# Kernel tuning notes

Hardware: AMD Instinct MI355X
Metric: run time of the kernel (lower is better)

## Reference

```python
import jax, jax.numpy as jnp
import numpy as np

NB_KERNEL = 100
DIM_PER_KERNEL = 5


def setup_inputs() -> dict:
    key = jax.random.key(0)
    k1, k2 = jax.random.split(key)
    B, F = 1024, 1024
    x = jax.random.normal(k1, (B, F), dtype=jnp.float32)
    T = jax.random.normal(k2, (F, NB_KERNEL * DIM_PER_KERNEL), dtype=jnp.float32)
    return {"x": x, "T": T}


def reference(x, T):
    B = x.shape[0]
    # project: [B, F] @ [F, K*D] -> [B, K, D]
    m = (x @ T).reshape(B, NB_KERNEL, DIM_PER_KERNEL)
    # pairwise L1 distance over D between all batch rows: [B, K, B]
    # diffs[i, k, d, j] = m[i, k, d] - m[j, k, d]
    diffs = m[:, :, :, None] - jnp.transpose(m, (1, 2, 0))[None, :, :, :]
    l1 = jnp.sum(jnp.abs(diffs), axis=2)  # [B, K, B]
    # exp-kernel similarity summed across batch (includes self term exp(0)=1)
    feat = jnp.sum(jnp.exp(-l1), axis=2)  # [B, K]
    return jnp.concatenate([x, feat], axis=1)  # [B, F + K]
```

## Files before the change

kernel.cpp:

```cpp
#include <hip/hip_runtime.h>
#include <hip/hip_bf16.h>
#include <math.h>

#define B_SZ   1024
#define F_SZ   1024
#define NKER   100
#define DKER   5
#define CCOLS  (NKER * DKER)
#define OUTW   (F_SZ + NKER)
#define LOG2E_F 1.44269504088896340736f

typedef __attribute__((ext_vector_type(8))) short bf16x8;
typedef __attribute__((ext_vector_type(4))) float f32x4;

__device__ __forceinline__ float exp2_hw(float x) {
    float r;
    asm("v_exp_f32 %0, %1" : "=v"(r) : "v"(x));
    return r;
}
__device__ __forceinline__ unsigned cvt_pk_bf16(float lo, float hi) {
    unsigned r;
    asm("v_cvt_pk_bf16_f32 %0, %1, %2" : "=v"(r) : "v"(lo), "v"(hi));
    return r;
}

__global__ __launch_bounds__(256) void init_kernel(const float* __restrict__ x,
                                                   float* __restrict__ out) {
    const int row = blockIdx.x;
    const int t = threadIdx.x;
    const float4 v = *reinterpret_cast<const float4*>(&x[row * F_SZ + t * 4]);
    *reinterpret_cast<float4*>(&out[row * OUTW + t * 4]) = v;
}

#define NCT 32
#define NJT (B_SZ / 16)

__global__ __launch_bounds__(256) void gemm_wave_kernel(const float* __restrict__ x,
                                                        const float* __restrict__ T,
                                                        float* __restrict__ mt) {
    const int tid = threadIdx.x;
    const int l = tid & 63;
    const int wv = tid >> 6;
    const int tile = blockIdx.x * 4 + wv;
    const int ct = tile & (NCT - 1);
    const int jt = tile >> 5;
    const int c0 = ct * 16, j0 = jt * 16;

    const int lr = l & 15;
    const int lk = (l >> 4) * 8;

    const int cA = c0 + lr;
    const int cL = (cA < CCOLS) ? cA : (CCOLS - 1);
    const int jB = j0 + lr;

    const float* ap = T + (size_t)lk * CCOLS + cL;
    const float* bp = x + (size_t)jB * F_SZ + lk;

    f32x4 acc = {0.f, 0.f, 0.f, 0.f};

    #pragma unroll 2
    for (int s = 0; s < F_SZ / 32; ++s) {
        const float a0 = ap[0 * CCOLS], a1 = ap[1 * CCOLS];
        const float a2 = ap[2 * CCOLS], a3 = ap[3 * CCOLS];
        const float a4 = ap[4 * CCOLS], a5 = ap[5 * CCOLS];
        const float a6 = ap[6 * CCOLS], a7 = ap[7 * CCOLS];
        const float4 b0 = *reinterpret_cast<const float4*>(bp);
        const float4 b1 = *reinterpret_cast<const float4*>(bp + 4);
        ap += 32 * CCOLS;
        bp += 32;

        union { unsigned u[4]; bf16x8 v; } A, B;
        A.u[0] = cvt_pk_bf16(a0, a1);
        A.u[1] = cvt_pk_bf16(a2, a3);
        A.u[2] = cvt_pk_bf16(a4, a5);
        A.u[3] = cvt_pk_bf16(a6, a7);
        B.u[0] = cvt_pk_bf16(b0.x, b0.y);
        B.u[1] = cvt_pk_bf16(b0.z, b0.w);
        B.u[2] = cvt_pk_bf16(b1.x, b1.y);
        B.u[3] = cvt_pk_bf16(b1.z, b1.w);

        acc = __builtin_amdgcn_mfma_f32_16x16x32_bf16(A.v, B.v, acc, 0, 0, 0);
    }

    const int jst = j0 + lr;
    const int cst = c0 + (l >> 4) * 4;
    #pragma unroll
    for (int q = 0; q < 4; ++q) {
        const int c = cst + q;
        if (c < CCOLS) mt[c * B_SZ + jst] = acc[q] * LOG2E_F;
    }
}

#define PJC 128

__global__ __launch_bounds__(64) void pair_kernel(const float* __restrict__ mt,
                                                  float* __restrict__ out) {
    __shared__ float mj[DKER * PJC];
    const int tid = threadIdx.x;
    const int i = blockIdx.x * 64 + tid;
    const int k = blockIdx.y;
    const int cb = k * DKER;

    const float a0 = mt[(cb + 0) * B_SZ + i];
    const float a1 = mt[(cb + 1) * B_SZ + i];
    const float a2 = mt[(cb + 2) * B_SZ + i];
    const float a3 = mt[(cb + 3) * B_SZ + i];
    const float a4 = mt[(cb + 4) * B_SZ + i];

    float acc = 0.f;
    for (int jc = 0; jc < B_SZ; jc += PJC) {
        __syncthreads();
        #pragma unroll
        for (int r = 0; r < DKER * PJC / 64; ++r) {
            const int t2 = r * 64 + tid;
            const int d = t2 >> 7;
            const int jr = t2 & (PJC - 1);
            mj[d * PJC + jr] = mt[(cb + d) * B_SZ + jc + jr];
        }
        __syncthreads();

        #pragma unroll 4
        for (int jb = 0; jb < PJC / 4; ++jb) {
            const float4 q0 = *reinterpret_cast<const float4*>(&mj[0 * PJC + jb * 4]);
            const float4 q1 = *reinterpret_cast<const float4*>(&mj[1 * PJC + jb * 4]);
            const float4 q2 = *reinterpret_cast<const float4*>(&mj[2 * PJC + jb * 4]);
            const float4 q3 = *reinterpret_cast<const float4*>(&mj[3 * PJC + jb * 4]);
            const float4 q4 = *reinterpret_cast<const float4*>(&mj[4 * PJC + jb * 4]);
#define DOJ(C) { \
            const float d0 = a0 - q0.C; \
            const float d1 = a1 - q1.C; \
            const float d2 = a2 - q2.C; \
            const float d3 = a3 - q3.C; \
            const float d4 = a4 - q4.C; \
            const float p01 = fabsf(d0) + fabsf(d1); \
            const float p23 = fabsf(d2) + fabsf(d3); \
            const float p234 = p23 + fabsf(d4); \
            acc += exp2_hw(-p01 - p234); }
            DOJ(x) DOJ(y) DOJ(z) DOJ(w)
#undef DOJ
        }
    }

    out[i * OUTW + F_SZ + k] = acc;
}

extern "C" void kernel_launch(void* const* d_in, const int* in_sizes, int n_in,
                              void* d_out, int out_size, void* d_ws, size_t ws_size,
                              hipStream_t stream) {
    const float* x = (const float*)d_in[0];
    const float* T = (const float*)d_in[1];
    float* out = (float*)d_out;
    float* mt = (float*)d_ws;

    init_kernel<<<dim3(B_SZ), 256, 0, stream>>>(x, out);
    gemm_wave_kernel<<<dim3(NCT * NJT / 4), 256, 0, stream>>>(x, T, mt);
    pair_kernel<<<dim3(B_SZ / 64, NKER), 64, 0, stream>>>(mt, out);
}
```

Before: 135.9 us.

## Share GEMM tiles via LDS with split-K and widen pair kernel blocks

The GEMM now gives each 512-thread block a 32x32 output tile. Operands are staged as bf16 in shared memory so four waves reuse them, and the K dimension is split across two half-blocks whose partial sums are combined through LDS. This removes the redundant, uncoalesced global loads of T that each wave issued separately. The pair kernel now uses 256 threads: it loads the full 5x1024 column slice into LDS once, each wave handles a quarter of the j range, and the partial sums are reduced in shared memory. The cost is more barriers and more LDS use per block, which may lower occupancy.

```diff
diff --git a/kernel.cpp b/kernel.cpp
--- a/kernel.cpp
+++ b/kernel.cpp
@@ -32,116 +32,127 @@
     *reinterpret_cast<float4*>(&out[row * OUTW + t * 4]) = v;
 }
 
-#define NCT 32
-#define NJT (B_SZ / 16)
+#define GAPAD 40
 
-__global__ __launch_bounds__(256) void gemm_wave_kernel(const float* __restrict__ x,
-                                                        const float* __restrict__ T,
-                                                        float* __restrict__ mt) {
+__global__ __launch_bounds__(512) void gemm_block_kernel(const float* __restrict__ x,
+                                                         const float* __restrict__ T,
+                                                         float* __restrict__ mt) {
+    __shared__ short Al[2][32][GAPAD];
+    __shared__ short Bl[2][32][GAPAD];
+    __shared__ float red[4][64][4];
     const int tid = threadIdx.x;
     const int l = tid & 63;
-    const int wv = tid >> 6;
-    const int tile = blockIdx.x * 4 + wv;
-    const int ct = tile & (NCT - 1);
-    const int jt = tile >> 5;
-    const int c0 = ct * 16, j0 = jt * 16;
+    const int w = tid >> 6;
+    const int h = tid >> 8;
+    const int ht = tid & 255;
+    const int c0 = blockIdx.x * 32;
+    const int j0 = blockIdx.y * 32;
+    const int fh = h * (F_SZ / 2);
 
-    const int lr = l & 15;
-    const int lk = (l >> 4) * 8;
+    const int sac = ht & 31;
+    const int sak = (ht >> 5) * 4;
+    const int cldA = (c0 + sac < CCOLS) ? (c0 + sac) : (CCOLS - 1);
+    const int sbj = ht >> 3;
+    const int sbk = (ht & 7) * 4;
 
-    const int cA = c0 + lr;
-    const int cL = (cA < CCOLS) ? cA : (CCOLS - 1);
-    const int jB = j0 + lr;
-
-    const float* ap = T + (size_t)lk * CCOLS + cL;
-    const float* bp = x + (size_t)jB * F_SZ + lk;
+    const int q = w & 3;
+    const int cq = (q & 1) * 16;
+    const int jq = (q >> 1) * 16;
+    const int fr = (l >> 4) * 8;
+    const int ar = cq + (l & 15);
+    const int br = jq + (l & 15);
 
     f32x4 acc = {0.f, 0.f, 0.f, 0.f};
 
-    #pragma unroll 2
-    for (int s = 0; s < F_SZ / 32; ++s) {
-        const float a0 = ap[0 * CCOLS], a1 = ap[1 * CCOLS];
-        const float a2 = ap[2 * CCOLS], a3 = ap[3 * CCOLS];
-        const float a4 = ap[4 * CCOLS], a5 = ap[5 * CCOLS];
-        const float a6 = ap[6 * CCOLS], a7 = ap[7 * CCOLS];
-        const float4 b0 = *reinterpret_cast<const float4*>(bp);
-        const float4 b1 = *reinterpret_cast<const float4*>(bp + 4);
-        ap += 32 * CCOLS;
-        bp += 32;
-
-        union { unsigned u[4]; bf16x8 v; } A, B;
-        A.u[0] = cvt_pk_bf16(a0, a1);
-        A.u[1] = cvt_pk_bf16(a2, a3);
-        A.u[2] = cvt_pk_bf16(a4, a5);
-        A.u[3] = cvt_pk_bf16(a6, a7);
-        B.u[0] = cvt_pk_bf16(b0.x, b0.y);
-        B.u[1] = cvt_pk_bf16(b0.z, b0.w);
-        B.u[2] = cvt_pk_bf16(b1.x, b1.y);
-        B.u[3] = cvt_pk_bf16(b1.z, b1.w);
-
-        acc = __builtin_amdgcn_mfma_f32_16x16x32_bf16(A.v, B.v, acc, 0, 0, 0);
+    for (int s = 0; s < 16; ++s) {
+        const int fb = fh + s * 32;
+        const float a0 = T[(fb + sak + 0) * CCOLS + cldA];
+        const float a1 = T[(fb + sak + 1) * CCOLS + cldA];
+        const float a2 = T[(fb + sak + 2) * CCOLS + cldA];
+        const float a3 = T[(fb + sak + 3) * CCOLS + cldA];
+        const float4 b = *reinterpret_cast<const float4*>(&x[(j0 + sbj) * F_SZ + fb + sbk]);
+        if (s) __syncthreads();
+        {
+            uint2 aw; aw.x = cvt_pk_bf16(a0, a1); aw.y = cvt_pk_bf16(a2, a3);
+            *reinterpret_cast<uint2*>(&Al[h][sac][sak]) = aw;
+            uint2 bw; bw.x = cvt_pk_bf16(b.x, b.y); bw.y = cvt_pk_bf16(b.z, b.w);
+            *reinterpret_cast<uint2*>(&Bl[h][sbj][sbk]) = bw;
+        }
+        __syncthreads();
+        const bf16x8 af = *reinterpret_cast<const bf16x8*>(&Al[h][ar][fr]);
+        const bf16x8 bf = *reinterpret_cast<const bf16x8*>(&Bl[h][br][fr]);
+        acc = __builtin_amdgcn_mfma_f32_16x16x32_bf16(af, bf, acc, 0, 0, 0);
     }
 
-    const int jst = j0 + lr;
-    const int cst = c0 + (l >> 4) * 4;
-    #pragma unroll
-    for (int q = 0; q < 4; ++q) {
-        const int c = cst + q;
-        if (c < CCOLS) mt[c * B_SZ + jst] = acc[q] * LOG2E_F;
+    if (h == 1) {
+        #pragma unroll
+        for (int qq = 0; qq < 4; ++qq) red[q][l][qq] = acc[qq];
+    }
+    __syncthreads();
+    if (h == 0) {
+        const int jst = j0 + jq + (l & 15);
+        const int cst = c0 + cq + (l >> 4) * 4;
+        #pragma unroll
+        for (int qq = 0; qq < 4; ++qq) {
+            const int c = cst + qq;
+            if (c < CCOLS)
+                mt[c * B_SZ + jst] = (acc[qq] + red[q][l][qq]) * LOG2E_F;
+        }
     }
 }
 
-#define PJC 128
-
-__global__ __launch_bounds__(64) void pair_kernel(const float* __restrict__ mt,
-                                                  float* __restrict__ out) {
-    __shared__ float mj[DKER * PJC];
+__global__ __launch_bounds__(256) void pair_kernel(const float* __restrict__ mt,
+                                                   float* __restrict__ out) {
+    __shared__ float mj[DKER][B_SZ];
+    __shared__ float red[256];
     const int tid = threadIdx.x;
-    const int i = blockIdx.x * 64 + tid;
+    const int bx = blockIdx.x;
     const int k = blockIdx.y;
     const int cb = k * DKER;
 
-    const float a0 = mt[(cb + 0) * B_SZ + i];
-    const float a1 = mt[(cb + 1) * B_SZ + i];
-    const float a2 = mt[(cb + 2) * B_SZ + i];
-    const float a3 = mt[(cb + 3) * B_SZ + i];
-    const float a4 = mt[(cb + 4) * B_SZ + i];
+    #pragma unroll
+    for (int d = 0; d < DKER; ++d) {
+        const float4 v = *reinterpret_cast<const float4*>(&mt[(cb + d) * B_SZ + tid * 4]);
+        *reinterpret_cast<float4*>(&mj[d][tid * 4]) = v;
+    }
+    __syncthreads();
+
+    const int lane = tid & 63;
+    const int w = tid >> 6;
+    const int i = bx * 64 + lane;
+    const float a0 = mj[0][i], a1 = mj[1][i], a2 = mj[2][i],
+                a3 = mj[3][i], a4 = mj[4][i];
 
     float acc = 0.f;
-    for (int jc = 0; jc < B_SZ; jc += PJC) {
-        __syncthreads();
-        #pragma unroll
-        for (int r = 0; r < DKER * PJC / 64; ++r) {
-            const int t2 = r * 64 + tid;
-            const int d = t2 >> 7;
-            const int jr = t2 & (PJC - 1);
-            mj[d * PJC + jr] = mt[(cb + d) * B_SZ + jc + jr];
-        }
-        __syncthreads();
-
-        #pragma unroll 4
-        for (int jb = 0; jb < PJC / 4; ++jb) {
-            const float4 q0 = *reinterpret_cast<const float4*>(&mj[0 * PJC + jb * 4]);
-            const float4 q1 = *reinterpret_cast<const float4*>(&mj[1 * PJC + jb * 4]);
-            const float4 q2 = *reinterpret_cast<const float4*>(&mj[2 * PJC + jb * 4]);
-            const float4 q3 = *reinterpret_cast<const float4*>(&mj[3 * PJC + jb * 4]);
-            const float4 q4 = *reinterpret_cast<const float4*>(&mj[4 * PJC + jb * 4]);
+    const int jbase = w * 256;
+    #pragma unroll 4
+    for (int jb = 0; jb < 64; ++jb) {
+        const int j4 = jbase + jb * 4;
+        const float4 q0 = *reinterpret_cast<const float4*>(&mj[0][j4]);
+        const float4 q1 = *reinterpret_cast<const float4*>(&mj[1][j4]);
+        const float4 q2 = *reinterpret_cast<const float4*>(&mj[2][j4]);
+        const float4 q3 = *reinterpret_cast<const float4*>(&mj[3][j4]);
+        const float4 q4 = *reinterpret_cast<const float4*>(&mj[4][j4]);
 #define DOJ(C) { \
-            const float d0 = a0 - q0.C; \
-            const float d1 = a1 - q1.C; \
-            const float d2 = a2 - q2.C; \
-            const float d3 = a3 - q3.C; \
-            const float d4 = a4 - q4.C; \
-            const float p01 = fabsf(d0) + fabsf(d1); \
-            const float p23 = fabsf(d2) + fabsf(d3); \
-            const float p234 = p23 + fabsf(d4); \
-            acc += exp2_hw(-p01 - p234); }
-            DOJ(x) DOJ(y) DOJ(z) DOJ(w)
+        const float d0 = a0 - q0.C; \
+        const float d1 = a1 - q1.C; \
+        const float d2 = a2 - q2.C; \
+        const float d3 = a3 - q3.C; \
+        const float d4 = a4 - q4.C; \
+        const float p01 = fabsf(d0) + fabsf(d1); \
+        const float p23 = fabsf(d2) + fabsf(d3); \
+        const float p234 = p23 + fabsf(d4); \
+        acc += exp2_hw(-p01 - p234); }
+        DOJ(x) DOJ(y) DOJ(z) DOJ(w)
 #undef DOJ
-        }
     }
 
-    out[i * OUTW + F_SZ + k] = acc;
+    red[tid] = acc;
+    __syncthreads();
+    if (tid < 64) {
+        const float s = red[tid] + red[tid + 64] + red[tid + 128] + red[tid + 192];
+        out[(bx * 64 + tid) * OUTW + F_SZ + k] = s;
+    }
 }
 
 extern "C" void kernel_launch(void* const* d_in, const int* in_sizes, int n_in,
@@ -153,6 +164,6 @@
     float* mt = (float*)d_ws;
 
     init_kernel<<<dim3(B_SZ), 256, 0, stream>>>(x, out);
-    gemm_wave_kernel<<<dim3(NCT * NJT / 4), 256, 0, stream>>>(x, T, mt);
-    pair_kernel<<<dim3(B_SZ / 64, NKER), 64, 0, stream>>>(mt, out);
+    gemm_block_kernel<<<dim3(16, 32), 512, 0, stream>>>(x, T, mt);
+    pair_kernel<<<dim3(B_SZ / 64, NKER), 256, 0, stream>>>(mt, out);
 }
```

New measurement: 111.9 us. -17.7%, faster.
